# Performance work log

Hardware: AMD Instinct MI355X
Metric: run time of the kernel (lower is better)

The kernel has to match this reference:

```python
import jax, jax.numpy as jnp
import numpy as np

SCALE = 8.0  # (dim // n_heads) ** 0.5 = (1024 // 16) ** 0.5


def setup_inputs() -> dict:
    key = jax.random.key(0)
    kq, kk, kv = jax.random.split(key, 3)
    shape = (2, 16, 2048, 64)  # [B, H, N, Dh]
    q = jax.random.normal(kq, shape, dtype=jnp.float32)
    k = jax.random.normal(kk, shape, dtype=jnp.float32)
    v = jax.random.normal(kv, shape, dtype=jnp.float32)
    return {"q": q, "k": k, "v": v}


def reference(q, k, v):
    # scores[b,h,n,m] = sum_d q[b,h,n,d] * k[b,h,m,d], then MULTIPLIED by scale
    # (the original multiplies by sqrt(head_dim), it does not divide).
    scores = jnp.einsum('bhnd,bhmd->bhnm', q, k) * SCALE
    scores = jax.nn.softmax(scores, axis=-1)
    # Faithful to the original quirky einsum: sums over n (query axis), keeps m.
    # out[b,h,m,d] = (sum_n scores[b,h,n,m]) * v[b,h,m,d]
    out = jnp.einsum('bhnm,bhmd->bhmd', scores, v)
    return out
```

## Files before the change

### kernel.cpp

```cpp
#include <hip/hip_runtime.h>
#include <math.h>

#define BH 32
#define NN 2048
#define DD 64
#define BHNN (BH * NN)
#define QK ((size_t)BH * NN * DD)

#define QSCALE 11.5415603f

typedef __attribute__((ext_vector_type(8)))  _Float16 halfx8;
typedef __attribute__((ext_vector_type(4)))  _Float16 halfx4;
typedef __attribute__((ext_vector_type(16))) float    floatx16;

__device__ inline float fexp2(float x) { return __builtin_amdgcn_exp2f(x); }

__device__ inline int rowmap(int r, int half) {
    return (r & 3) + 8 * (r >> 2) + 4 * half;
}

__global__ __launch_bounds__(256) void convert_kernel(const float4* __restrict__ q,
                                                      const float4* __restrict__ k,
                                                      _Float16* __restrict__ qhi,
                                                      _Float16* __restrict__ qlo,
                                                      _Float16* __restrict__ khi) {
    size_t gid = (size_t)blockIdx.x * 256 + threadIdx.x;
    float4 qa = q[gid];
    float4 ka = k[gid];
    float qf[4] = {qa.x, qa.y, qa.z, qa.w};
    float kf[4] = {ka.x, ka.y, ka.z, ka.w};
    halfx4 h, l, kh;
#pragma unroll
    for (int i = 0; i < 4; ++i) {
        float f = qf[i] * QSCALE;
        _Float16 hh = (_Float16)f;
        h[i] = hh;
        l[i] = (_Float16)(f - (float)hh);
        kh[i] = (_Float16)kf[i];
    }
    *(halfx4*)&qhi[gid * 4] = h;
    *(halfx4*)&qlo[gid * 4] = l;
    size_t rowbase = (gid * 4) & ~(size_t)63;
    int j = (int)((gid >> 1) & 7) ^ (int)((gid >> 4) & 7);
    *(halfx4*)&khi[rowbase + (size_t)(j << 3) + ((gid & 1) << 2)] = kh;
}

__device__ inline void stage_tile_async(const _Float16* __restrict__ gtile,
                                        _Float16* lds, int wave, int lane) {
#pragma unroll
    for (int i = 0; i < 4; ++i) {
        const char* gp = (const char*)gtile + wave * 4096 + i * 1024 + lane * 16;
        char* lp = (char*)lds + wave * 4096 + i * 1024;
        __builtin_amdgcn_global_load_lds(
            (const __attribute__((address_space(1))) unsigned int*)gp,
            (__attribute__((address_space(3))) unsigned int*)lp, 16, 0, 0);
    }
}

__device__ inline void load_a(const _Float16* __restrict__ qhi_row,
                              const _Float16* __restrict__ qlo_row,
                              int half, halfx8 ah[4], halfx8 al[4]) {
#pragma unroll
    for (int ks = 0; ks < 4; ++ks) {
        ah[ks] = *(const halfx8*)&qhi_row[ks * 16 + half * 8];
        al[ks] = *(const halfx8*)&qlo_row[ks * 16 + half * 8];
    }
}

__global__ __launch_bounds__(256, 3) void stats_kernel(const _Float16* __restrict__ qhi,
                                                       const _Float16* __restrict__ qlo,
                                                       const _Float16* __restrict__ khi,
                                                       float* __restrict__ smax_p,
                                                       float* __restrict__ sden_p) {
    __shared__ _Float16 K2[2 * 128 * 64];
    const int g    = blockIdx.x & 63;
    const int bh   = g & 31;
    const int ms   = g >> 5;
    const int n0   = (blockIdx.x >> 6) * 128;
    const int tid  = threadIdx.x;
    const int wave = tid >> 6, lane = tid & 63;
    const int half = lane >> 5, l31 = lane & 31;
    const int xr   = l31 & 7;
    const size_t base = (size_t)bh * NN * DD;

    const _Float16* khi_b = khi + base;
    stage_tile_async(khi_b + (size_t)(ms * 8) * 8192, K2, wave, lane);

    halfx8 ah[4], al[4];
    {
        size_t ro = base + (size_t)(n0 + wave * 32 + l31) * DD;
        load_a(qhi + ro, qlo + ro, half, ah, al);
    }

    float m_run[16], d_run[16];
#pragma unroll
    for (int r = 0; r < 16; ++r) { m_run[r] = -INFINITY; d_run[r] = 0.f; }

    __syncthreads();

    for (int mti = 0; mti < 8; ++mti) {
        const _Float16* Kc = K2 + (mti & 1) * 8192;
        if (mti < 7)
            stage_tile_async(khi_b + (size_t)(ms * 8 + mti + 1) * 8192,
                             K2 + ((mti + 1) & 1) * 8192, wave, lane);

        floatx16 acc[4];
#pragma unroll
        for (int t = 0; t < 4; ++t)
#pragma unroll
            for (int e = 0; e < 16; ++e) acc[t][e] = 0.f;

#pragma unroll
        for (int t = 0; t < 4; ++t) {
            const int mr = t * 32 + l31;
            const _Float16* rowp = Kc + (size_t)mr * 64;
#pragma unroll
            for (int ks = 0; ks < 4; ++ks) {
                const int j = (ks * 2 + half) ^ xr;
                halfx8 bhf = *(const halfx8*)&rowp[j << 3];
                acc[t] = __builtin_amdgcn_mfma_f32_32x32x16_f16(ah[ks], bhf, acc[t], 0, 0, 0);
                acc[t] = __builtin_amdgcn_mfma_f32_32x32x16_f16(al[ks], bhf, acc[t], 0, 0, 0);
            }
        }

#pragma unroll
        for (int r = 0; r < 16; ++r) {
            float tmax = fmaxf(fmaxf(acc[0][r], acc[1][r]), fmaxf(acc[2][r], acc[3][r]));
            float m_new = fmaxf(m_run[r], tmax);
            float s = fexp2(acc[0][r] - m_new) + fexp2(acc[1][r] - m_new)
                    + fexp2(acc[2][r] - m_new) + fexp2(acc[3][r] - m_new);
            d_run[r] = d_run[r] * fexp2(m_run[r] - m_new) + s;
            m_run[r] = m_new;
        }

        if (mti < 7) __syncthreads();
    }

    float* smp = smax_p + ((size_t)ms * BH + bh) * NN;
    float* sdp = sden_p + ((size_t)ms * BH + bh) * NN;
#pragma unroll
    for (int r = 0; r < 16; ++r) {
        float M = m_run[r];
#pragma unroll
        for (int off = 1; off < 32; off <<= 1)
            M = fmaxf(M, __shfl_xor(M, off));
        float dd = d_run[r] * fexp2(m_run[r] - M);
#pragma unroll
        for (int off = 1; off < 32; off <<= 1)
            dd += __shfl_xor(dd, off);
        if (l31 == 0) {
            int row = n0 + wave * 32 + rowmap(r, half);
            smp[row] = M;
            sdp[row] = dd;
        }
    }
}

__global__ __launch_bounds__(256, 3) void wsum_kernel(const _Float16* __restrict__ qhi,
                                                      const _Float16* __restrict__ qlo,
                                                      const _Float16* __restrict__ khi,
                                                      const float* __restrict__ smax_p,
                                                      const float* __restrict__ sden_p,
                                                      float* __restrict__ wpart) {
    __shared__ _Float16 Khi[128 * 64];
    __shared__ float wred[4 * 128];
    __shared__ float Ms[1024];
    __shared__ float Is[1024];
    const int g    = blockIdx.x & 63;
    const int bh   = g & 31;
    const int nz   = g >> 5;
    const int m0   = (blockIdx.x >> 6) * 128;
    const int tid  = threadIdx.x;
    const int wave = tid >> 6, lane = tid & 63;
    const int half = lane >> 5, l31 = lane & 31;
    const int xr   = l31 & 7;
    const size_t base = (size_t)bh * NN * DD;

    stage_tile_async(khi + base + (size_t)m0 * 64, Khi, wave, lane);

    {
        size_t roff = (size_t)bh * NN + nz * 1024 + tid * 4;
        float4 m0v = *(const float4*)&smax_p[roff];
        float4 m1v = *(const float4*)&smax_p[(size_t)BHNN + roff];
        float4 d0v = *(const float4*)&sden_p[roff];
        float4 d1v = *(const float4*)&sden_p[(size_t)BHNN + roff];
        float mm0[4] = {m0v.x, m0v.y, m0v.z, m0v.w};
        float mm1[4] = {m1v.x, m1v.y, m1v.z, m1v.w};
        float dd0[4] = {d0v.x, d0v.y, d0v.z, d0v.w};
        float dd1[4] = {d1v.x, d1v.y, d1v.z, d1v.w};
#pragma unroll
        for (int j = 0; j < 4; ++j) {
            float M = fmaxf(mm0[j], mm1[j]);
            float den = dd0[j] * fexp2(mm0[j] - M) + dd1[j] * fexp2(mm1[j] - M);
            Ms[tid * 4 + j] = M;
            Is[tid * 4 + j] = 1.0f / den;
        }
    }
    __syncthreads();

    float wacc[4] = {0.f, 0.f, 0.f, 0.f};

#pragma unroll
    for (int it = 0; it < 8; ++it) {
        const int ls = wave + it * 4;
        halfx8 ah[4], al[4];
        {
            size_t ro = base + (size_t)((nz * 32 + ls) * 32 + l31) * DD;
            load_a(qhi + ro, qlo + ro, half, ah, al);
        }

        floatx16 acc[4];
#pragma unroll
        for (int t = 0; t < 4; ++t)
#pragma unroll
            for (int e = 0; e < 16; ++e) acc[t][e] = 0.f;

#pragma unroll
        for (int t = 0; t < 4; ++t) {
            const int mr = t * 32 + l31;
            const _Float16* rowp = Khi + (size_t)mr * 64;
#pragma unroll
            for (int ks = 0; ks < 4; ++ks) {
                const int j = (ks * 2 + half) ^ xr;
                halfx8 bhf = *(const halfx8*)&rowp[j << 3];
                acc[t] = __builtin_amdgcn_mfma_f32_32x32x16_f16(ah[ks], bhf, acc[t], 0, 0, 0);
                acc[t] = __builtin_amdgcn_mfma_f32_32x32x16_f16(al[ks], bhf, acc[t], 0, 0, 0);
            }
        }

#pragma unroll
        for (int r = 0; r < 16; ++r) {
            const int lrow = ls * 32 + rowmap(r, half);
            float M   = Ms[lrow];
            float inv = Is[lrow];
#pragma unroll
            for (int t = 0; t < 4; ++t)
                wacc[t] += fexp2(acc[t][r] - M) * inv;
        }
    }

#pragma unroll
    for (int t = 0; t < 4; ++t) wacc[t] += __shfl_xor(wacc[t], 32);
    if (half == 0) {
#pragma unroll
        for (int t = 0; t < 4; ++t) wred[wave * 128 + t * 32 + l31] = wacc[t];
    }
    __syncthreads();
    if (tid < 128) {
        float s = wred[tid] + wred[128 + tid] + wred[256 + tid] + wred[384 + tid];
        wpart[((size_t)nz * BH + bh) * NN + m0 + tid] = s;
    }
}

__global__ __launch_bounds__(256) void out_kernel(const float* __restrict__ v,
                                                  const float* __restrict__ w0,
                                                  const float* __restrict__ w1,
                                                  float* __restrict__ out) {
    size_t gid = (size_t)blockIdx.x * 256 + threadIdx.x;
    const float4* v4 = (const float4*)v;
    float4* o4 = (float4*)out;
    float4 vv = v4[gid];
    float ww = w0[gid >> 4] + w1[gid >> 4];
    o4[gid] = make_float4(vv.x * ww, vv.y * ww, vv.z * ww, vv.w * ww);
}

extern "C" void kernel_launch(void* const* d_in, const int* in_sizes, int n_in,
                              void* d_out, int out_size, void* d_ws, size_t ws_size,
                              hipStream_t stream) {
    const float* q = (const float*)d_in[0];
    const float* k = (const float*)d_in[1];
    const float* v = (const float*)d_in[2];
    float* out = (float*)d_out;

    _Float16* qhi = (_Float16*)d_ws;
    _Float16* qlo = qhi + QK;
    _Float16* khi = qlo + QK;
    float* smax_p = (float*)(khi + QK);
    float* sden_p = smax_p + 2 * BHNN;
    float* wpart  = sden_p + 2 * BHNN;

    convert_kernel<<<QK / 4 / 256, 256, 0, stream>>>((const float4*)q, (const float4*)k,
                                                     qhi, qlo, khi);
    stats_kernel<<<1024, 256, 0, stream>>>(qhi, qlo, khi, smax_p, sden_p);
    wsum_kernel<<<1024, 256, 0, stream>>>(qhi, qlo, khi, smax_p, sden_p, wpart);
    out_kernel<<<(BH * NN * DD / 4) / 256, 256, 0, stream>>>(v, wpart, wpart + BHNN, out);
}
```

Measured before the change: 192.5 us.

## Split MFMA tiles into halves to raise occupancy and fold inverse denominator into max

Both the stats and wsum kernels now process each 128-column K tile in two halves of 64 columns, with only two 32x32 accumulators live at a time and non-unrolled loops. Launch bounds rise from 3 to 4 blocks per CU, which cuts register pressure. In wsum, the reciprocal denominator is folded into the subtracted max as log2(den), which removes the Is shared array and one multiply per element. The trade-off is less instruction-level parallelism per wave, extra loop overhead, and slightly different rounding from the log/exp2 path.

```diff
diff --git a/kernel.cpp b/kernel.cpp
--- a/kernel.cpp
+++ b/kernel.cpp
@@ -14,6 +14,7 @@
 typedef __attribute__((ext_vector_type(16))) float    floatx16;
 
 __device__ inline float fexp2(float x) { return __builtin_amdgcn_exp2f(x); }
+__device__ inline float flog2(float x) { return __builtin_amdgcn_logf(x); }
 
 __device__ inline int rowmap(int r, int half) {
     return (r & 3) + 8 * (r >> 2) + 4 * half;
@@ -67,7 +68,7 @@
     }
 }
 
-__global__ __launch_bounds__(256, 3) void stats_kernel(const _Float16* __restrict__ qhi,
+__global__ __launch_bounds__(256, 4) void stats_kernel(const _Float16* __restrict__ qhi,
                                                        const _Float16* __restrict__ qlo,
                                                        const _Float16* __restrict__ khi,
                                                        float* __restrict__ smax_p,
@@ -98,39 +99,42 @@
 
     __syncthreads();
 
+#pragma unroll 1
     for (int mti = 0; mti < 8; ++mti) {
         const _Float16* Kc = K2 + (mti & 1) * 8192;
         if (mti < 7)
             stage_tile_async(khi_b + (size_t)(ms * 8 + mti + 1) * 8192,
                              K2 + ((mti + 1) & 1) * 8192, wave, lane);
 
-        floatx16 acc[4];
-#pragma unroll
-        for (int t = 0; t < 4; ++t)
-#pragma unroll
-            for (int e = 0; e < 16; ++e) acc[t][e] = 0.f;
-
-#pragma unroll
-        for (int t = 0; t < 4; ++t) {
-            const int mr = t * 32 + l31;
-            const _Float16* rowp = Kc + (size_t)mr * 64;
-#pragma unroll
-            for (int ks = 0; ks < 4; ++ks) {
-                const int j = (ks * 2 + half) ^ xr;
-                halfx8 bhf = *(const halfx8*)&rowp[j << 3];
-                acc[t] = __builtin_amdgcn_mfma_f32_32x32x16_f16(ah[ks], bhf, acc[t], 0, 0, 0);
-                acc[t] = __builtin_amdgcn_mfma_f32_32x32x16_f16(al[ks], bhf, acc[t], 0, 0, 0);
-            }
-        }
-
-#pragma unroll
-        for (int r = 0; r < 16; ++r) {
-            float tmax = fmaxf(fmaxf(acc[0][r], acc[1][r]), fmaxf(acc[2][r], acc[3][r]));
-            float m_new = fmaxf(m_run[r], tmax);
-            float s = fexp2(acc[0][r] - m_new) + fexp2(acc[1][r] - m_new)
-                    + fexp2(acc[2][r] - m_new) + fexp2(acc[3][r] - m_new);
-            d_run[r] = d_run[r] * fexp2(m_run[r] - m_new) + s;
-            m_run[r] = m_new;
+#pragma unroll 1
+        for (int p = 0; p < 2; ++p) {
+            floatx16 acc[2];
+#pragma unroll
+            for (int t = 0; t < 2; ++t)
+#pragma unroll
+                for (int e = 0; e < 16; ++e) acc[t][e] = 0.f;
+
+#pragma unroll
+            for (int tt = 0; tt < 2; ++tt) {
+                const int mr = (p * 2 + tt) * 32 + l31;
+                const _Float16* rowp = Kc + (size_t)mr * 64;
+#pragma unroll
+                for (int ks = 0; ks < 4; ++ks) {
+                    const int j = (ks * 2 + half) ^ xr;
+                    halfx8 bhf = *(const halfx8*)&rowp[j << 3];
+                    acc[tt] = __builtin_amdgcn_mfma_f32_32x32x16_f16(ah[ks], bhf, acc[tt], 0, 0, 0);
+                    acc[tt] = __builtin_amdgcn_mfma_f32_32x32x16_f16(al[ks], bhf, acc[tt], 0, 0, 0);
+                }
+            }
+
+#pragma unroll
+            for (int r = 0; r < 16; ++r) {
+                float tmax = fmaxf(acc[0][r], acc[1][r]);
+                float m_new = fmaxf(m_run[r], tmax);
+                float s = fexp2(acc[0][r] - m_new) + fexp2(acc[1][r] - m_new);
+                d_run[r] = d_run[r] * fexp2(m_run[r] - m_new) + s;
+                m_run[r] = m_new;
+            }
         }
 
         if (mti < 7) __syncthreads();
@@ -156,7 +160,7 @@
     }
 }
 
-__global__ __launch_bounds__(256, 3) void wsum_kernel(const _Float16* __restrict__ qhi,
+__global__ __launch_bounds__(256, 4) void wsum_kernel(const _Float16* __restrict__ qhi,
                                                       const _Float16* __restrict__ qlo,
                                                       const _Float16* __restrict__ khi,
                                                       const float* __restrict__ smax_p,
@@ -165,7 +169,6 @@
     __shared__ _Float16 Khi[128 * 64];
     __shared__ float wred[4 * 128];
     __shared__ float Ms[1024];
-    __shared__ float Is[1024];
     const int g    = blockIdx.x & 63;
     const int bh   = g & 31;
     const int nz   = g >> 5;
@@ -192,15 +195,14 @@
         for (int j = 0; j < 4; ++j) {
             float M = fmaxf(mm0[j], mm1[j]);
             float den = dd0[j] * fexp2(mm0[j] - M) + dd1[j] * fexp2(mm1[j] - M);
-            Ms[tid * 4 + j] = M;
-            Is[tid * 4 + j] = 1.0f / den;
+            Ms[tid * 4 + j] = M + flog2(den);
         }
     }
     __syncthreads();
 
-    float wacc[4] = {0.f, 0.f, 0.f, 0.f};
-
-#pragma unroll
+    float wacc0 = 0.f, wacc1 = 0.f, wacc2 = 0.f, wacc3 = 0.f;
+
+#pragma unroll 1
     for (int it = 0; it < 8; ++it) {
         const int ls = wave + it * 4;
         halfx8 ah[4], al[4];
@@ -209,36 +211,41 @@
             load_a(qhi + ro, qlo + ro, half, ah, al);
         }
 
-        floatx16 acc[4];
-#pragma unroll
-        for (int t = 0; t < 4; ++t)
-#pragma unroll
-            for (int e = 0; e < 16; ++e) acc[t][e] = 0.f;
-
-#pragma unroll
-        for (int t = 0; t < 4; ++t) {
-            const int mr = t * 32 + l31;
-            const _Float16* rowp = Khi + (size_t)mr * 64;
-#pragma unroll
-            for (int ks = 0; ks < 4; ++ks) {
-                const int j = (ks * 2 + half) ^ xr;
-                halfx8 bhf = *(const halfx8*)&rowp[j << 3];
-                acc[t] = __builtin_amdgcn_mfma_f32_32x32x16_f16(ah[ks], bhf, acc[t], 0, 0, 0);
-                acc[t] = __builtin_amdgcn_mfma_f32_32x32x16_f16(al[ks], bhf, acc[t], 0, 0, 0);
-            }
-        }
-
-#pragma unroll
-        for (int r = 0; r < 16; ++r) {
-            const int lrow = ls * 32 + rowmap(r, half);
-            float M   = Ms[lrow];
-            float inv = Is[lrow];
-#pragma unroll
-            for (int t = 0; t < 4; ++t)
-                wacc[t] += fexp2(acc[t][r] - M) * inv;
-        }
-    }
-
+#pragma unroll 1
+        for (int p = 0; p < 2; ++p) {
+            floatx16 acc[2];
+#pragma unroll
+            for (int t = 0; t < 2; ++t)
+#pragma unroll
+                for (int e = 0; e < 16; ++e) acc[t][e] = 0.f;
+
+#pragma unroll
+            for (int tt = 0; tt < 2; ++tt) {
+                const int mr = (p * 2 + tt) * 32 + l31;
+                const _Float16* rowp = Khi + (size_t)mr * 64;
+#pragma unroll
+                for (int ks = 0; ks < 4; ++ks) {
+                    const int j = (ks * 2 + half) ^ xr;
+                    halfx8 bhf = *(const halfx8*)&rowp[j << 3];
+                    acc[tt] = __builtin_amdgcn_mfma_f32_32x32x16_f16(ah[ks], bhf, acc[tt], 0, 0, 0);
+                    acc[tt] = __builtin_amdgcn_mfma_f32_32x32x16_f16(al[ks], bhf, acc[tt], 0, 0, 0);
+                }
+            }
+
+            float w0 = 0.f, w1 = 0.f;
+#pragma unroll
+            for (int r = 0; r < 16; ++r) {
+                const int lrow = ls * 32 + rowmap(r, half);
+                float Madj = Ms[lrow];
+                w0 += fexp2(acc[0][r] - Madj);
+                w1 += fexp2(acc[1][r] - Madj);
+            }
+            if (p == 0) { wacc0 += w0; wacc1 += w1; }
+            else        { wacc2 += w0; wacc3 += w1; }
+        }
+    }
+
+    float wacc[4] = {wacc0, wacc1, wacc2, wacc3};
 #pragma unroll
     for (int t = 0; t < 4; ++t) wacc[t] += __shfl_xor(wacc[t], 32);
     if (half == 0) {
```

New measurement: 188.7 us. -2.0%, faster.
